# Kernel optimization log

Measured on AMD Instinct MI355X. Metric: run time of the kernel, lower is better.

Reference implementation:

```python
import jax, jax.numpy as jnp
import numpy as np

B, N, K, D = 8, 4096, 16, 256


def layer_norm(x, g, b, eps=1e-5):
    m = jnp.mean(x, axis=-1, keepdims=True)
    v = jnp.var(x, axis=-1, keepdims=True)
    return (x - m) * jax.lax.rsqrt(v + eps) * g + b


def setup_inputs() -> dict:
    key = jax.random.key(0)
    ks = jax.random.split(key, 8)

    def lin(k, fi, fo):
        return (jax.random.normal(k, (fi, fo), jnp.float32) / np.sqrt(fi).astype(np.float32),
                jnp.zeros((fo,), jnp.float32))

    coordinates = jax.random.normal(ks[0], (B, N, 3), jnp.float32)
    W1, b1 = lin(ks[1], 10, D // 4)
    W2, b2 = lin(ks[2], D // 4, D // 2)
    W3, b3 = lin(ks[3], D // 2, D)
    Wa1, ba1 = lin(ks[4], D, D)
    Wa2, ba2 = lin(ks[5], D, D)
    return {
        'coordinates': coordinates,
        'W1': W1, 'b1': b1, 'g1': jnp.ones((D // 4,)), 'be1': jnp.zeros((D // 4,)),
        'W2': W2, 'b2': b2, 'g2': jnp.ones((D // 2,)), 'be2': jnp.zeros((D // 2,)),
        'W3': W3, 'b3': b3, 'g3': jnp.ones((D,)), 'be3': jnp.zeros((D,)),
        'Wa1': Wa1, 'ba1': ba1, 'ga1': jnp.ones((D,)), 'bea1': jnp.zeros((D,)),
        'Wa2': Wa2, 'ba2': ba2,
    }


def reference(coordinates, W1, b1, g1, be1, W2, b2, g2, be2, W3, b3, g3, be3,
              Wa1, ba1, ga1, bea1, Wa2, ba2):
    # kNN via squared-distance matrix (monotone in Euclidean distance)
    sq = jnp.sum(coordinates * coordinates, axis=-1)  # [B,N]
    d2 = sq[:, :, None] + sq[:, None, :] - 2.0 * jnp.einsum('bnd,bmd->bnm', coordinates, coordinates)
    _, idx = jax.lax.top_k(-d2, K)  # smallest K distances, [B,N,K]

    nbr = jax.vmap(lambda c, i: c[i])(coordinates, idx)  # [B,N,K,3]
    rel = nbr - coordinates[:, :, None, :]               # relative positions
    dist = jnp.linalg.norm(rel, axis=-1, keepdims=True)  # [B,N,K,1]
    rn = rel / (dist + 1e-6)
    axy = jnp.arctan2(rn[..., 1], rn[..., 0])[..., None]
    axz = jnp.arctan2(rn[..., 2], rn[..., 0])[..., None]
    ayz = jnp.arctan2(rn[..., 2], rn[..., 1])[..., None]
    geom = jnp.concatenate([dist, rel, axy, axz, ayz, rn], axis=-1)  # [B,N,K,10]

    # encoder MLP
    h = jax.nn.relu(layer_norm(geom @ W1 + b1, g1, be1))
    h = jax.nn.relu(layer_norm(h @ W2 + b2, g2, be2))
    h = layer_norm(h @ W3 + b3, g3, be3)

    agg = jnp.mean(h, axis=2)  # mean over neighbors -> [B,N,D]

    # aggregator MLP
    out = jax.nn.relu(layer_norm(agg @ Wa1 + ba1, ga1, bea1)) @ Wa2 + ba2
    return out
```

## Files before the change

### kernel.cpp

```cpp
#include <hip/hip_runtime.h>
#include <hip/hip_bf16.h>
#include <math.h>

#define BB 8
#define NN 4096
#define KK 16
#define DD 256

typedef __hip_bfloat16 bf16;
typedef _Float16 half8 __attribute__((ext_vector_type(8)));
typedef float f32x4 __attribute__((ext_vector_type(4)));

union HFU { _Float16 h; unsigned short u; };
__device__ __forceinline__ unsigned short f2h(float x) { HFU v; v.h = (_Float16)x; return v.u; }

#define CONV_TOTAL 273344
#define O_COORD 0
#define O_W1 98304
#define O_b1 98944
#define O_g1 99008
#define O_be1 99072
#define O_W2 99136
#define O_b2 107328
#define O_g2 107456
#define O_be2 107584
#define O_W3 107712
#define O_b3 140480
#define O_g3 140736
#define O_be3 140992
#define O_Wa1 141248
#define O_ba1 206784
#define O_ga1 207040
#define O_bea1 207296
#define O_Wa2 207552
#define O_ba2 273088

#define F_W1 0
#define F_W2 2048
#define F_W3 10240
#define F_A1 43008
#define F_A2 108544
#define FRAG_TOTAL 174080

struct SrcPtrs {
  const void* p[19];
};

__global__ __launch_bounds__(256) void convert_kernel(SrcPtrs sp, float* __restrict__ dst) {
  static constexpr int OFF[20] = {
      0,      98304,  98944,  99008,  99072,  99136,  107328, 107456, 107584,
      107712, 140480, 140736, 140992, 141248, 206784, 207040, 207296, 207552,
      273088, 273344};
  const int i = blockIdx.x * 256 + threadIdx.x;
  if (i >= CONV_TOTAL) return;
  const unsigned tag = ((const unsigned*)sp.p[3])[0];
  const bool isb = (tag == 0x3F803F80u);
  int s = 0;
#pragma unroll
  for (int j = 1; j < 19; j++)
    if (i >= OFF[j]) s = j;
  const int local = i - OFF[s];
  float v = isb ? __bfloat162float(((const bf16*)sp.p[s])[local])
                : ((const float*)sp.p[s])[local];
  dst[i] = v;
}

__global__ __launch_bounds__(256) void swizzle_kernel(const float* __restrict__ conv,
                                                      unsigned short* __restrict__ frag) {
  const int t = blockIdx.x * 256 + threadIdx.x;
  if (t >= FRAG_TOTAL) return;
  int l, e;
  if (t < 2048) { l = 0; e = t; }
  else if (t < 10240) { l = 1; e = t - 2048; }
  else if (t < 43008) { l = 2; e = t - 10240; }
  else if (t < 108544) { l = 3; e = t - 43008; }
  else { l = 4; e = t - 108544; }
  static constexpr int WOFF[5] = {O_W1, O_W2, O_W3, O_Wa1, O_Wa2};
  static constexpr int NDIM[5] = {64, 128, 256, 256, 256};
  static constexpr int NTC[5] = {4, 8, 16, 16, 16};
  static constexpr int KREAL[5] = {10, 64, 128, 256, 256};
  static constexpr int HOFF[5] = {F_W1, F_W2, F_W3, F_A1, F_A2};
  const int j = e & 7;
  const int lane = (e >> 3) & 63;
  const int tile = e >> 9;
  const int nt = tile % NTC[l];
  const int kt = tile / NTC[l];
  const int k = kt * 32 + (lane >> 4) * 8 + j;
  const int n = nt * 16 + (lane & 15);
  float w = (k < KREAL[l]) ? conv[WOFF[l] + k * NDIM[l] + n] : 0.0f;
  frag[HOFF[l] + e] = f2h(w);
}

__device__ __forceinline__ float sq3_rn(float x, float y, float z) {
  return __fadd_rn(__fadd_rn(__fmul_rn(x, x), __fmul_rn(y, y)), __fmul_rn(z, z));
}
__device__ __forceinline__ float dot3_rn(float ax, float ay, float az, float bx, float by, float bz) {
  return __fadd_rn(__fadd_rn(__fmul_rn(ax, bx), __fmul_rn(ay, by)), __fmul_rn(az, bz));
}
__device__ __forceinline__ unsigned f2ord(float f) {
  unsigned u = __float_as_uint(f);
  return (u & 0x80000000u) ? ~u : (u | 0x80000000u);
}
__device__ __forceinline__ float ord2f(unsigned o) {
  unsigned u = (o & 0x80000000u) ? (o & 0x7FFFFFFFu) : ~o;
  return __uint_as_float(u);
}

__global__ __launch_bounds__(256) void prep_kernel(const float* __restrict__ conv,
                                                   float4* __restrict__ soa) {
  const int i = blockIdx.x * 256 + threadIdx.x;
  if (i >= BB * NN) return;
  const float* c = conv + O_COORD + (size_t)i * 3;
  float x = c[0], y = c[1], z = c[2];
  soa[i] = make_float4(x, y, z, sq3_rn(x, y, z));
}

__global__ __launch_bounds__(256) void knn_wave_kernel(const float4* __restrict__ soa,
                                                       int* __restrict__ idx_out) {
  const int lane = threadIdx.x & 63;
  const int wid = (blockIdx.x * 256 + threadIdx.x) >> 6;
  const int q0 = wid * 4;
  const int b = q0 >> 12;
  const float4* P = soa + (size_t)b * NN;

  float cx[4], cy[4], cz[4], sqn[4];
#pragma unroll
  for (int j = 0; j < 4; j++) {
    float4 c = P[(q0 + j) & (NN - 1)];
    cx[j] = c.x; cy[j] = c.y; cz[j] = c.z; sqn[j] = c.w;
  }

  unsigned long long R[4];
  float tauf[4];

  float4 c0 = P[lane];
  float4 cnext = P[64 + lane];

#pragma unroll
  for (int j = 0; j < 4; j++) {
    float dot = dot3_rn(cx[j], cy[j], cz[j], c0.x, c0.y, c0.z);
    float d2 = __fsub_rn(__fadd_rn(sqn[j], c0.w), __fmul_rn(2.0f, dot));
    unsigned long long key = (((unsigned long long)f2ord(d2)) << 32) | (unsigned)lane;
#pragma unroll
    for (int k = 2; k <= 64; k <<= 1) {
#pragma unroll
      for (int jj = k >> 1; jj > 0; jj >>= 1) {
        unsigned long long v = __shfl_xor(key, jj, 64);
        bool asc = ((lane & k) == 0);
        bool up = ((lane & jj) != 0);
        unsigned long long mn = (key < v) ? key : v;
        unsigned long long mx2 = (key < v) ? v : key;
        key = (up == asc) ? mx2 : mn;
      }
    }
    R[j] = key;
    tauf[j] = ord2f((unsigned)(__shfl(R[j], 15, 64) >> 32));
  }

  for (int bt = 1; bt < 64; bt++) {
    const float4 c = cnext;
    if (bt < 63) cnext = P[(bt + 1) * 64 + lane];
    const int m0 = bt * 64;
    float d2v[4];
    unsigned long long pm[4];
#pragma unroll
    for (int j = 0; j < 4; j++) {
      float dot = dot3_rn(cx[j], cy[j], cz[j], c.x, c.y, c.z);
      d2v[j] = __fsub_rn(__fadd_rn(sqn[j], c.w), __fmul_rn(2.0f, dot));
      pm[j] = __ballot(d2v[j] <= tauf[j]);
    }
    if (pm[0] | pm[1] | pm[2] | pm[3]) {
#pragma unroll
      for (int j = 0; j < 4; j++) {
        unsigned long long pmask = pm[j];
        if (pmask) {
          do {
            int s = __builtin_ctzll(pmask);
            pmask &= pmask - 1;
            float d2s = __shfl(d2v[j], s, 64);
            unsigned long long nk =
                (((unsigned long long)f2ord(d2s)) << 32) | (unsigned)(m0 + s);
            unsigned long long lt = __ballot(R[j] < nk) & 0xFFFFull;
            int pos = __builtin_popcountll(lt);
            unsigned long long prev = __shfl_up(R[j], 1, 64);
            if (lane == pos) R[j] = nk;
            else if (lane > pos) R[j] = prev;
          } while (pmask);
          tauf[j] = ord2f((unsigned)(__shfl(R[j], 15, 64) >> 32));
        }
      }
    }
  }

#pragma unroll
  for (int j = 0; j < 4; j++)
    if (lane < KK)
      idx_out[(size_t)(q0 + j) * KK + lane] = (int)(R[j] & 0xFFFFFFFFull);
}

template <int KT>
__device__ __forceinline__ void load_afrags(half8* A, const unsigned short* lF,
                                            int rowe, int lane) {
#pragma unroll
  for (int kt = 0; kt < KT; kt++) {
    int off = (lane & 15) * rowe + kt * 32 + (lane >> 4) * 8;
    A[kt] = *reinterpret_cast<const half8*>(lF + off);
  }
}

template <int NT>
__device__ __forceinline__ void init_acc(f32x4* acc, const float* __restrict__ bias,
                                         int lane) {
  const int col = lane & 15;
#pragma unroll
  for (int nt = 0; nt < NT; nt++) {
    float bv = bias[nt * 16 + col];
    acc[nt] = {bv, bv, bv, bv};
  }
}

template <int KT, int NT>
__device__ __forceinline__ void gemm_acc(f32x4* acc, const half8* A,
                                         const unsigned short* bb, int lane) {
#pragma unroll
  for (int kt = 0; kt < KT; kt++)
#pragma unroll
    for (int nt = 0; nt < NT; nt++) {
      const half8 bf = *reinterpret_cast<const half8*>(bb + (kt * NT + nt) * 512 + lane * 8);
      acc[nt] = __builtin_amdgcn_mfma_f32_16x16x32_f16(A[kt], bf, acc[nt], 0, 0, 0);
    }
}

template <int NT>
__device__ __forceinline__ void ln_stats(const f32x4* acc, float* m, float* rs) {
  float s[4] = {0.f, 0.f, 0.f, 0.f}, s2[4] = {0.f, 0.f, 0.f, 0.f};
#pragma unroll
  for (int nt = 0; nt < NT; nt++)
#pragma unroll
    for (int r = 0; r < 4; r++) {
      float v = acc[nt][r];
      s[r] += v;
      s2[r] += v * v;
    }
#pragma unroll
  for (int msk = 1; msk <= 8; msk <<= 1)
#pragma unroll
    for (int r = 0; r < 4; r++) {
      s[r] += __shfl_xor(s[r], msk, 64);
      s2[r] += __shfl_xor(s2[r], msk, 64);
    }
  const float invN = 1.0f / (NT * 16);
#pragma unroll
  for (int r = 0; r < 4; r++) {
    m[r] = s[r] * invN;
    float var = s2[r] * invN - m[r] * m[r];
    rs[r] = rsqrtf(var + 1e-5f);
  }
}

template <int NT, bool RELU>
__device__ __forceinline__ void ln_store(const f32x4* acc, const float* m, const float* rs,
                                         const float* __restrict__ g, const float* __restrict__ be,
                                         unsigned short* lF, int rowe, int lane) {
  const int col = lane & 15;
  const int rbase = (lane >> 4) * 4;
#pragma unroll
  for (int nt = 0; nt < NT; nt++) {
    float gv = g[nt * 16 + col], bv = be[nt * 16 + col];
#pragma unroll
    for (int r = 0; r < 4; r++) {
      float v = (acc[nt][r] - m[r]) * rs[r] * gv + bv;
      if (RELU) v = fmaxf(v, 0.0f);
      lF[(rbase + r) * rowe + nt * 16 + col] = f2h(v);
    }
  }
}

__device__ __forceinline__ void stage_b(unsigned short* bbuf,
                                        const unsigned short* __restrict__ src,
                                        int n_u4, int tid) {
  const uint4* s = reinterpret_cast<const uint4*>(src);
  uint4* d = reinterpret_cast<uint4*>(bbuf);
  for (int i = tid; i < n_u4; i += 256) d[i] = s[i];
}

#define ROWE_E 136
#define PSTR_E (16 * ROWE_E)

__global__ __launch_bounds__(256, 3) void encoder_mfma(
    const float* __restrict__ conv, const int* __restrict__ nbr,
    const unsigned short* __restrict__ frag, unsigned short* __restrict__ agF) {
  __shared__ unsigned short planes[4 * PSTR_E];
  __shared__ unsigned short Bbuf[16384];
  const int tid = threadIdx.x;
  const int lane = tid & 63;
  const int wave = tid >> 6;
  const int point = blockIdx.x * 4 + wave;
  const int b = point >> 12;
  const int n = point & (NN - 1);
  const float* cb = conv + O_COORD + (size_t)b * NN * 3;
  unsigned short* lF = planes + wave * PSTR_E;

  {
    int pl = tid >> 6, row = (tid >> 2) & 15, part = tid & 3;
    *reinterpret_cast<uint4*>(planes + pl * PSTR_E + row * ROWE_E + part * 8) =
        make_uint4(0u, 0u, 0u, 0u);
    stage_b(Bbuf, frag + F_W1, 1280, tid);
  }
  __syncthreads();

  if (lane < 16) {
    float cx = cb[n * 3 + 0], cy = cb[n * 3 + 1], cz = cb[n * 3 + 2];
    int id = nbr[(size_t)point * KK + lane];
    float rx = __fsub_rn(cb[id * 3 + 0], cx);
    float ry = __fsub_rn(cb[id * 3 + 1], cy);
    float rz = __fsub_rn(cb[id * 3 + 2], cz);
    float dist = __fsqrt_rn(sq3_rn(rx, ry, rz));
    float den = __fadd_rn(dist, 1e-6f);
    float ux = __fdiv_rn(rx, den), uy = __fdiv_rn(ry, den), uz = __fdiv_rn(rz, den);
    float ge[10];
    ge[0] = dist; ge[1] = rx; ge[2] = ry; ge[3] = rz;
    ge[4] = atan2f(uy, ux); ge[5] = atan2f(uz, ux); ge[6] = atan2f(uz, uy);
    ge[7] = ux; ge[8] = uy; ge[9] = uz;
#pragma unroll
    for (int c = 0; c < 10; c++) lF[lane * ROWE_E + c] = f2h(ge[c]);
  }

  float m[4], rs[4];
  {
    half8 A[1];
    load_afrags<1>(A, lF, ROWE_E, lane);
    f32x4 acc[4];
    init_acc<4>(acc, conv + O_b1, lane);
    gemm_acc<1, 4>(acc, A, Bbuf, lane);
    ln_stats<4>(acc, m, rs);
    ln_store<4, true>(acc, m, rs, conv + O_g1, conv + O_be1, lF, ROWE_E, lane);
  }
  {
    half8 A[2];
    load_afrags<2>(A, lF, ROWE_E, lane);
    f32x4 acc[8];
    init_acc<8>(acc, conv + O_b2, lane);
    gemm_acc<2, 8>(acc, A, Bbuf + 2048, lane);
    ln_stats<8>(acc, m, rs);
    ln_store<8, true>(acc, m, rs, conv + O_g2, conv + O_be2, lF, ROWE_E, lane);
  }
  half8 A3[4];
  load_afrags<4>(A3, lF, ROWE_E, lane);
  f32x4 acc[16];
  init_acc<16>(acc, conv + O_b3, lane);
  __syncthreads();
  stage_b(Bbuf, frag + F_W3, 2048, tid);
  __syncthreads();
  gemm_acc<2, 16>(acc, A3, Bbuf, lane);
  __syncthreads();
  stage_b(Bbuf, frag + F_W3 + 16384, 2048, tid);
  __syncthreads();
  gemm_acc<2, 16>(acc, A3 + 2, Bbuf, lane);

  {
    ln_stats<16>(acc, m, rs);
    const int col = lane & 15;
    float sv[16];
#pragma unroll
    for (int nt = 0; nt < 16; nt++) {
      float gv = conv[O_g3 + nt * 16 + col], bv = conv[O_be3 + nt * 16 + col];
      float s = 0.f;
#pragma unroll
      for (int r = 0; r < 4; r++) s += (acc[nt][r] - m[r]) * rs[r] * gv + bv;
      s += __shfl_xor(s, 16, 64);
      s += __shfl_xor(s, 32, 64);
      sv[nt] = s * (1.0f / 16.0f);
    }
    if (lane < 16) {
      size_t base = (size_t)point * DD;
#pragma unroll
      for (int nt = 0; nt < 16; nt++) agF[base + nt * 16 + lane] = f2h(sv[nt]);
    }
  }
}

#define ROWE_A 264

__global__ __launch_bounds__(256) void aggmlp_mfma(
    const float* __restrict__ conv, const unsigned short* __restrict__ agF,
    const unsigned short* __restrict__ a1, const unsigned short* __restrict__ a2,
    const unsigned* __restrict__ g1raw, void* __restrict__ out) {
  __shared__ unsigned short lds[4][16 * ROWE_A];
  const int lane = threadIdx.x & 63;
  const int wave = threadIdx.x >> 6;
  const int row0 = (blockIdx.x * 4 + wave) * 16;
  unsigned short* lF = lds[wave];

#pragma unroll
  for (int t = 0; t < 8; t++) {
    int v = t * 64 + lane;
    int row = v >> 5;
    int c0 = (v & 31) * 8;
    *reinterpret_cast<uint4*>(lF + row * ROWE_A + c0) =
        *reinterpret_cast<const uint4*>(agF + ((size_t)(row0 + row) * DD + c0));
  }
  __syncthreads();

  float m[4], rs[4];
  f32x4 acc[16];
  {
    half8 A[8];
    load_afrags<8>(A, lF, ROWE_A, lane);
    init_acc<16>(acc, conv + O_ba1, lane);
    gemm_acc<8, 16>(acc, A, a1, lane);
    ln_stats<16>(acc, m, rs);
    ln_store<16, true>(acc, m, rs, conv + O_ga1, conv + O_bea1, lF, ROWE_A, lane);
  }
  __syncthreads();
  {
    half8 A[8];
    load_afrags<8>(A, lF, ROWE_A, lane);
    init_acc<16>(acc, conv + O_ba2, lane);
    gemm_acc<8, 16>(acc, A, a2, lane);
  }
  const bool isb = (g1raw[0] == 0x3F803F80u);
  const int col = lane & 15;
  const int rbase = (lane >> 4) * 4;
  if (isb) {
    bf16* o = (bf16*)out;
#pragma unroll
    for (int nt = 0; nt < 16; nt++)
#pragma unroll
      for (int r = 0; r < 4; r++)
        o[(size_t)(row0 + rbase + r) * DD + nt * 16 + col] = __float2bfloat16(acc[nt][r]);
  } else {
    float* o = (float*)out;
#pragma unroll
    for (int nt = 0; nt < 16; nt++)
#pragma unroll
      for (int r = 0; r < 4; r++)
        o[(size_t)(row0 + rbase + r) * DD + nt * 16 + col] = acc[nt][r];
  }
}

extern "C" void kernel_launch(void* const* d_in, const int* in_sizes, int n_in,
                              void* d_out, int out_size, void* d_ws, size_t ws_size,
                              hipStream_t stream) {
  char* ws = (char*)d_ws;
  float* conv = (float*)ws;
  int* idx_ws = (int*)(ws + 1093376);
  unsigned short* agF = (unsigned short*)(ws + 3190528);
  unsigned short* frag = (unsigned short*)(ws + 19967744);
  float4* soa = (float4*)(ws + 20315904);

  SrcPtrs sp;
  for (int i = 0; i < 19; i++) sp.p[i] = d_in[i];

  convert_kernel<<<(CONV_TOTAL + 255) / 256, 256, 0, stream>>>(sp, conv);
  swizzle_kernel<<<(FRAG_TOTAL + 255) / 256, 256, 0, stream>>>(conv, frag);
  prep_kernel<<<(BB * NN + 255) / 256, 256, 0, stream>>>(conv, soa);

  knn_wave_kernel<<<BB * NN / 16, 256, 0, stream>>>(soa, idx_ws);

  encoder_mfma<<<BB * NN / 4, 256, 0, stream>>>(conv, idx_ws, frag, agF);

  aggmlp_mfma<<<BB * NN / 64, 256, 0, stream>>>(conv, agF, frag + F_A1, frag + F_A2,
                                                (const unsigned*)d_in[3], d_out);
}
```

Before: 422.0 us.

## Use FMA prefilter with margin in kNN scan, prefetch W3 via registers

The kNN scan now computes an approximate squared distance with three FMAs on pre-scaled (-2x) coordinates and screens candidates against the threshold plus a small margin. Admitted candidates get their exact rounded distance recomputed, so the selected set should match the reference. The encoder also loads both halves of W3 into registers ahead of the LDS stores, so the second half's global load overlaps the first GEMM. This costs an extra soa buffer, more registers, and some extra candidate insertions caused by the margin.

New measurement: 583.8 us. 1.38x slower.

```diff
diff --git a/kernel.cpp b/kernel.cpp
--- a/kernel.cpp
+++ b/kernel.cpp
@@ -107,21 +107,28 @@
 }
 
 __global__ __launch_bounds__(256) void prep_kernel(const float* __restrict__ conv,
-                                                   float4* __restrict__ soa) {
+                                                   float4* __restrict__ soa,
+                                                   float4* __restrict__ soas) {
   const int i = blockIdx.x * 256 + threadIdx.x;
   if (i >= BB * NN) return;
   const float* c = conv + O_COORD + (size_t)i * 3;
   float x = c[0], y = c[1], z = c[2];
-  soa[i] = make_float4(x, y, z, sq3_rn(x, y, z));
-}
+  float sq = sq3_rn(x, y, z);
+  soa[i] = make_float4(x, y, z, sq);
+  soas[i] = make_float4(-2.0f * x, -2.0f * y, -2.0f * z, sq);
+}
+
+#define D2_MARGIN 2e-4f
 
 __global__ __launch_bounds__(256) void knn_wave_kernel(const float4* __restrict__ soa,
+                                                       const float4* __restrict__ soas,
                                                        int* __restrict__ idx_out) {
   const int lane = threadIdx.x & 63;
   const int wid = (blockIdx.x * 256 + threadIdx.x) >> 6;
   const int q0 = wid * 4;
   const int b = q0 >> 12;
   const float4* P = soa + (size_t)b * NN;
+  const float4* PS = soas + (size_t)b * NN;
 
   float cx[4], cy[4], cz[4], sqn[4];
 #pragma unroll
@@ -131,43 +138,48 @@
   }
 
   unsigned long long R[4];
-  float tauf[4];
-
-  float4 c0 = P[lane];
-  float4 cnext = P[64 + lane];
-
-#pragma unroll
-  for (int j = 0; j < 4; j++) {
-    float dot = dot3_rn(cx[j], cy[j], cz[j], c0.x, c0.y, c0.z);
-    float d2 = __fsub_rn(__fadd_rn(sqn[j], c0.w), __fmul_rn(2.0f, dot));
-    unsigned long long key = (((unsigned long long)f2ord(d2)) << 32) | (unsigned)lane;
-#pragma unroll
-    for (int k = 2; k <= 64; k <<= 1) {
-#pragma unroll
-      for (int jj = k >> 1; jj > 0; jj >>= 1) {
-        unsigned long long v = __shfl_xor(key, jj, 64);
-        bool asc = ((lane & k) == 0);
-        bool up = ((lane & jj) != 0);
-        unsigned long long mn = (key < v) ? key : v;
-        unsigned long long mx2 = (key < v) ? v : key;
-        key = (up == asc) ? mx2 : mn;
+  float tauf[4], taum[4];
+
+  float4 cnext = PS[64 + lane];
+
+  {
+    const float4 c0 = P[lane];
+#pragma unroll
+    for (int j = 0; j < 4; j++) {
+      float dot = dot3_rn(cx[j], cy[j], cz[j], c0.x, c0.y, c0.z);
+      float d2 = __fsub_rn(__fadd_rn(sqn[j], c0.w), __fmul_rn(2.0f, dot));
+      unsigned long long key = (((unsigned long long)f2ord(d2)) << 32) | (unsigned)lane;
+#pragma unroll
+      for (int k = 2; k <= 64; k <<= 1) {
+#pragma unroll
+        for (int jj = k >> 1; jj > 0; jj >>= 1) {
+          unsigned long long v = __shfl_xor(key, jj, 64);
+          bool asc = ((lane & k) == 0);
+          bool up = ((lane & jj) != 0);
+          unsigned long long mn = (key < v) ? key : v;
+          unsigned long long mx2 = (key < v) ? v : key;
+          key = (up == asc) ? mx2 : mn;
+        }
       }
-    }
-    R[j] = key;
-    tauf[j] = ord2f((unsigned)(__shfl(R[j], 15, 64) >> 32));
+      R[j] = key;
+      tauf[j] = ord2f((unsigned)(__shfl(R[j], 15, 64) >> 32));
+      taum[j] = tauf[j] + D2_MARGIN;
+    }
   }
 
   for (int bt = 1; bt < 64; bt++) {
     const float4 c = cnext;
-    if (bt < 63) cnext = P[(bt + 1) * 64 + lane];
+    if (bt < 63) cnext = PS[(bt + 1) * 64 + lane];
     const int m0 = bt * 64;
-    float d2v[4];
+    float d2a[4];
     unsigned long long pm[4];
 #pragma unroll
     for (int j = 0; j < 4; j++) {
-      float dot = dot3_rn(cx[j], cy[j], cz[j], c.x, c.y, c.z);
-      d2v[j] = __fsub_rn(__fadd_rn(sqn[j], c.w), __fmul_rn(2.0f, dot));
-      pm[j] = __ballot(d2v[j] <= tauf[j]);
+      float s = c.w + sqn[j];
+      float t = fmaf(c.z, cz[j], s);
+      t = fmaf(c.y, cy[j], t);
+      d2a[j] = fmaf(c.x, cx[j], t);
+      pm[j] = __ballot(d2a[j] <= taum[j]);
     }
     if (pm[0] | pm[1] | pm[2] | pm[3]) {
 #pragma unroll
@@ -177,9 +189,14 @@
           do {
             int s = __builtin_ctzll(pmask);
             pmask &= pmask - 1;
-            float d2s = __shfl(d2v[j], s, 64);
+            float mx = -0.5f * __shfl(c.x, s, 64);
+            float my = -0.5f * __shfl(c.y, s, 64);
+            float mz = -0.5f * __shfl(c.z, s, 64);
+            float msq = __shfl(c.w, s, 64);
+            float dot = dot3_rn(cx[j], cy[j], cz[j], mx, my, mz);
+            float d2e = __fsub_rn(__fadd_rn(sqn[j], msq), __fmul_rn(2.0f, dot));
             unsigned long long nk =
-                (((unsigned long long)f2ord(d2s)) << 32) | (unsigned)(m0 + s);
+                (((unsigned long long)f2ord(d2e)) << 32) | (unsigned)(m0 + s);
             unsigned long long lt = __ballot(R[j] < nk) & 0xFFFFull;
             int pos = __builtin_popcountll(lt);
             unsigned long long prev = __shfl_up(R[j], 1, 64);
@@ -187,6 +204,7 @@
             else if (lane > pos) R[j] = prev;
           } while (pmask);
           tauf[j] = ord2f((unsigned)(__shfl(R[j], 15, 64) >> 32));
+          taum[j] = tauf[j] + D2_MARGIN;
         }
       }
     }
@@ -330,31 +348,48 @@
   {
     half8 A[1];
     load_afrags<1>(A, lF, ROWE_E, lane);
-    f32x4 acc[4];
-    init_acc<4>(acc, conv + O_b1, lane);
-    gemm_acc<1, 4>(acc, A, Bbuf, lane);
-    ln_stats<4>(acc, m, rs);
-    ln_store<4, true>(acc, m, rs, conv + O_g1, conv + O_be1, lF, ROWE_E, lane);
+    f32x4 acc1[4];
+    init_acc<4>(acc1, conv + O_b1, lane);
+    gemm_acc<1, 4>(acc1, A, Bbuf, lane);
+    ln_stats<4>(acc1, m, rs);
+    ln_store<4, true>(acc1, m, rs, conv + O_g1, conv + O_be1, lF, ROWE_E, lane);
   }
   {
     half8 A[2];
     load_afrags<2>(A, lF, ROWE_E, lane);
-    f32x4 acc[8];
-    init_acc<8>(acc, conv + O_b2, lane);
-    gemm_acc<2, 8>(acc, A, Bbuf + 2048, lane);
-    ln_stats<8>(acc, m, rs);
-    ln_store<8, true>(acc, m, rs, conv + O_g2, conv + O_be2, lF, ROWE_E, lane);
-  }
+    f32x4 acc2[8];
+    init_acc<8>(acc2, conv + O_b2, lane);
+    gemm_acc<2, 8>(acc2, A, Bbuf + 2048, lane);
+    ln_stats<8>(acc2, m, rs);
+    ln_store<8, true>(acc2, m, rs, conv + O_g2, conv + O_be2, lF, ROWE_E, lane);
+  }
+
   half8 A3[4];
   load_afrags<4>(A3, lF, ROWE_E, lane);
   f32x4 acc[16];
   init_acc<16>(acc, conv + O_b3, lane);
-  __syncthreads();
-  stage_b(Bbuf, frag + F_W3, 2048, tid);
+
+  const uint4* w3s = reinterpret_cast<const uint4*>(frag + F_W3);
+  uint4 r0[8];
+#pragma unroll
+  for (int i = 0; i < 8; i++) r0[i] = w3s[tid + i * 256];
+  __syncthreads();
+  {
+    uint4* d = reinterpret_cast<uint4*>(Bbuf);
+#pragma unroll
+    for (int i = 0; i < 8; i++) d[tid + i * 256] = r0[i];
+  }
+  uint4 r1[8];
+#pragma unroll
+  for (int i = 0; i < 8; i++) r1[i] = w3s[2048 + tid + i * 256];
   __syncthreads();
   gemm_acc<2, 16>(acc, A3, Bbuf, lane);
   __syncthreads();
-  stage_b(Bbuf, frag + F_W3 + 16384, 2048, tid);
+  {
+    uint4* d = reinterpret_cast<uint4*>(Bbuf);
+#pragma unroll
+    for (int i = 0; i < 8; i++) d[tid + i * 256] = r1[i];
+  }
   __syncthreads();
   gemm_acc<2, 16>(acc, A3 + 2, Bbuf, lane);
 
@@ -448,15 +483,16 @@
   unsigned short* agF = (unsigned short*)(ws + 3190528);
   unsigned short* frag = (unsigned short*)(ws + 19967744);
   float4* soa = (float4*)(ws + 20315904);
+  float4* soas = (float4*)(ws + 20840192);
 
   SrcPtrs sp;
   for (int i = 0; i < 19; i++) sp.p[i] = d_in[i];
 
   convert_kernel<<<(CONV_TOTAL + 255) / 256, 256, 0, stream>>>(sp, conv);
   swizzle_kernel<<<(FRAG_TOTAL + 255) / 256, 256, 0, stream>>>(conv, frag);
-  prep_kernel<<<(BB * NN + 255) / 256, 256, 0, stream>>>(conv, soa);
-
-  knn_wave_kernel<<<BB * NN / 16, 256, 0, stream>>>(soa, idx_ws);
+  prep_kernel<<<(BB * NN + 255) / 256, 256, 0, stream>>>(conv, soa, soas);
+
+  knn_wave_kernel<<<BB * NN / 16, 256, 0, stream>>>(soa, soas, idx_ws);
 
   encoder_mfma<<<BB * NN / 4, 256, 0, stream>>>(conv, idx_ws, frag, agF);
 
```
